# Performance work log

Measured on AMD Instinct MI355X. Metric: run time of the kernel, lower is better.

## Reference

```python
import jax, jax.numpy as jnp
import numpy as np

T, H, E, K, I = 2048, 2048, 64, 8, 768
CAP = 512


def setup_inputs() -> dict:
    key = jax.random.key(0)
    ks = jax.random.split(key, 5)
    s = 0.02
    return {
        "hidden_states": jax.random.normal(ks[0], (T, H), jnp.float32),
        "w_router": jax.random.normal(ks[1], (E, H), jnp.float32) * s,
        "w_gate": jax.random.normal(ks[2], (E, H, I), jnp.float32) * s,
        "w_up": jax.random.normal(ks[3], (E, H, I), jnp.float32) * s,
        "w_down": jax.random.normal(ks[4], (E, I, H), jnp.float32) * s,
    }


def _moe(x, w_router, w_gate, w_up, w_down):
    Tn = x.shape[0]
    # --- router: softmax -> top-k -> renormalize (norm_topk_prob=True) ---
    logits = x @ w_router.T                                   # [T, E]
    probs = jax.nn.softmax(logits.astype(jnp.float32), axis=-1)
    topk_w, topk_idx = jax.lax.top_k(probs, K)                # [T, K]
    topk_w = topk_w / jnp.sum(topk_w, axis=-1, keepdims=True)
    # --- dispatch: sort (token, expert) pairs by expert, scatter into capacity buffers ---
    e = topk_idx.reshape(-1)                                  # [T*K] expert id per pair
    t = jnp.repeat(jnp.arange(Tn), K)                         # [T*K] token id per pair
    w = topk_w.reshape(-1)                                    # [T*K] combine weight per pair
    order = jnp.argsort(e, stable=True)
    e_s, t_s, w_s = e[order], t[order], w[order]
    counts = jax.ops.segment_sum(jnp.ones_like(e_s), e_s, num_segments=E)  # [E]
    starts = jnp.cumsum(counts) - counts                      # start offset of each expert group
    pos = jnp.arange(Tn * K) - starts[e_s]                    # slot within expert
    valid = pos < CAP
    posc = jnp.where(valid, pos, 0)
    vm = valid.astype(x.dtype)[:, None]
    buf = jnp.zeros((E, CAP, H), x.dtype).at[e_s, posc].add(x[t_s] * vm)   # [E, C, H]
    # --- grouped expert SwiGLU FFN: down(silu(gate(x)) * up(x)) ---
    g = jnp.einsum('ech,ehi->eci', buf, w_gate)               # [E, C, I]
    u = jnp.einsum('ech,ehi->eci', buf, w_up)                 # [E, C, I]
    y = jnp.einsum('eci,eih->ech', jax.nn.silu(g) * u, w_down)  # [E, C, H]
    # --- combine: gather expert outputs back to tokens, weighted sum ---
    gw = (w_s.astype(x.dtype) * valid.astype(x.dtype))[:, None]
    out = jnp.zeros((Tn, H), x.dtype).at[t_s].add(gw * y[e_s, posc])
    return out


def reference(hidden_states, w_router, w_gate, w_up, w_down):
    return _moe(hidden_states, w_router, w_gate, w_up, w_down)
```

## Files before the change

kernel.cpp:

```cpp
#include <hip/hip_runtime.h>
#include <hip/hip_bf16.h>
#include <math.h>

#define T_TOK 2048
#define H_DIM 2048
#define NEXP  64
#define TOPK  8
#define I_DIM 768
#define CAPE  512
#define MTMAX 4
#define LDW   40

typedef short bf16x8 __attribute__((ext_vector_type(8)));
typedef float f32x4  __attribute__((ext_vector_type(4)));

__device__ __forceinline__ unsigned short f2bf(float f) {
  unsigned u = __float_as_uint(f);
  u += 0x7fffu + ((u >> 16) & 1u);
  return (unsigned short)(u >> 16);
}
__device__ __forceinline__ float bf2f(unsigned short b) {
  return __uint_as_float(((unsigned)b) << 16);
}
__device__ __forceinline__ unsigned pack2(float lo, float hi) {
  __hip_bfloat162 h = __float22bfloat162_rn(make_float2(lo, hi));
  unsigned r; __builtin_memcpy(&r, &h, 4); return r;
}

__global__ __launch_bounds__(256) void k_xcvt(const float* __restrict__ x,
                                              unsigned short* __restrict__ xb) {
  const size_t i = ((size_t)blockIdx.x * 256 + threadIdx.x) * 8;
  float4 p = *(const float4*)(x + i);
  float4 q = *(const float4*)(x + i + 4);
  union { unsigned u[4]; bf16x8 v; } r;
  r.u[0] = pack2(p.x, p.y); r.u[1] = pack2(p.z, p.w);
  r.u[2] = pack2(q.x, q.y); r.u[3] = pack2(q.z, q.w);
  *(bf16x8*)(xb + i) = r.v;
}

__global__ __launch_bounds__(256) void k_router(const float* __restrict__ x,
                                                const float* __restrict__ wr,
                                                int* __restrict__ topk_idx,
                                                float* __restrict__ topk_w) {
  const int lane = threadIdx.x & 63;
  const int t = blockIdx.x * 4 + (threadIdx.x >> 6);
  const float4* xr   = (const float4*)(x + (size_t)t * H_DIM);
  const float4* wrow = (const float4*)(wr + (size_t)lane * H_DIM);
  float acc = 0.f;
  for (int i = 0; i < H_DIM / 4; ++i) {
    float4 a = xr[i], b = wrow[i];
    acc = fmaf(a.x, b.x, acc); acc = fmaf(a.y, b.y, acc);
    acc = fmaf(a.z, b.z, acc); acc = fmaf(a.w, b.w, acc);
  }
  float cur = acc;
  float val[TOPK]; int idx[TOPK];
#pragma unroll
  for (int r = 0; r < TOPK; ++r) {
    float bv = cur; int bi = lane;
#pragma unroll
    for (int off = 32; off > 0; off >>= 1) {
      float ov = __shfl_xor(bv, off);
      int   oi = __shfl_xor(bi, off);
      if (ov > bv || (ov == bv && oi < bi)) { bv = ov; bi = oi; }
    }
    val[r] = bv; idx[r] = bi;
    if (lane == bi) cur = -INFINITY;
  }
  float m = val[0], s = 0.f, w[TOPK];
#pragma unroll
  for (int r = 0; r < TOPK; ++r) { w[r] = expf(val[r] - m); s += w[r]; }
  if (lane < TOPK) {
    topk_idx[t * TOPK + lane] = idx[lane];
    topk_w [t * TOPK + lane] = w[lane] / s;
  }
}

__global__ __launch_bounds__(1024) void k_rank(const int* __restrict__ topk_idx,
                                               int* __restrict__ pair_pos,
                                               int* __restrict__ slot_token,
                                               int* __restrict__ cnts) {
  __shared__ int s_run[64];
  __shared__ int s_whist[16][64];
  const int tid = threadIdx.x, lane = tid & 63, wv = tid >> 6;
  const int sub = wv >> 2;
  if (tid < 64) s_run[tid] = 0;
  for (int it = 0; it < 16; ++it) {
    const int p = (it * 4 + sub) * 256 + (tid & 255);
    const int e = topk_idx[p];
    __syncthreads();
    s_whist[wv][lane] = 0;
    __syncthreads();
    unsigned long long m = ~0ull;
#pragma unroll
    for (int b = 0; b < 6; ++b) {
      unsigned long long bb = __ballot((e >> b) & 1);
      m &= ((e >> b) & 1) ? bb : ~bb;
    }
    const int rw = __popcll(m & ((1ull << lane) - 1ull));
    if (rw == 0) s_whist[wv][e] = __popcll(m);
    __syncthreads();
    int off = rw;
    for (int w2 = 0; w2 < wv; ++w2) off += s_whist[w2][e];
    const int pos = s_run[e] + off;
    pair_pos[p] = pos;
    if (pos < CAPE) slot_token[e * CAPE + pos] = p >> 3;
    __syncthreads();
    if (tid < 64) {
      int tsum = 0;
#pragma unroll
      for (int w2 = 0; w2 < 16; ++w2) tsum += s_whist[w2][tid];
      s_run[tid] += tsum;
    }
  }
  __syncthreads();
  if (tid < 64) cnts[tid] = s_run[tid];
}

__global__ __launch_bounds__(512) void k_gateup(const unsigned short* __restrict__ xb,
                                                const float* __restrict__ wg,
                                                const float* __restrict__ wu,
                                                const int* __restrict__ slot_token,
                                                const int* __restrict__ cnts,
                                                unsigned short* __restrict__ act) {
  const int NB = NEXP * MTMAX * 6;
  const int v = (blockIdx.x & 7) * (NB / 8) + (blockIdx.x >> 3);
  const int e = v / (MTMAX * 6);
  const int rem = v % (MTMAX * 6);
  const int mt = rem / 6, nt = rem % 6;

  int cnt = cnts[e]; cnt = cnt < CAPE ? cnt : CAPE;
  if (cnt <= 0 || mt * 128 >= cnt) return;
  const int m0 = mt << 7;

  __shared__ __align__(16) short As[2][128 * LDW];
  __shared__ __align__(16) short Bg[2][128 * LDW];
  __shared__ __align__(16) short Bu[2][128 * LDW];

  const int tid = threadIdx.x;
  const int lane = tid & 63, wave = tid >> 6;
  const int wm = wave >> 2, wn = wave & 3;
  const int lr = lane & 15, lg = lane >> 4;

  const int a_row = tid >> 2, a_ko = (tid & 3) * 8;
  const int b_mat = tid >> 8;
  const int b_idx = tid & 255;
  const int b_kq = b_idx & 7, b_nq = b_idx >> 3;
  const size_t wbase = (size_t)e * H_DIM * I_DIM + (size_t)nt * 128;

  const int tok = (m0 + a_row < cnt) ? slot_token[e * CAPE + m0 + a_row] : 0;
  const unsigned short* xr = xb + (size_t)tok * H_DIM + a_ko;
  const float* bp  = (b_mat ? wu : wg) + wbase + (size_t)(4 * b_kq) * I_DIM + 4 * b_nq;
  short* Bdst0 = b_mat ? Bu[0] : Bg[0];
  short* Bdst1 = b_mat ? Bu[1] : Bg[1];

  f32x4 accg[4][2], accu[4][2];
#pragma unroll
  for (int mi = 0; mi < 4; ++mi)
#pragma unroll
    for (int ni = 0; ni < 2; ++ni) {
      accg[mi][ni] = (f32x4){0.f, 0.f, 0.f, 0.f};
      accu[mi][ni] = (f32x4){0.f, 0.f, 0.f, 0.f};
    }

  struct Tile { bf16x8 a; float4 b[4]; };

  auto LOAD = [&](Tile& Tl, int kt) {
    const int k0 = kt * 32;
    Tl.a = *(const bf16x8*)(xr + k0);
    const float* r0 = bp + (size_t)k0 * I_DIM;
#pragma unroll
    for (int j = 0; j < 4; ++j)
      Tl.b[j] = *(const float4*)(r0 + (size_t)j * I_DIM);
  };
  auto STORE = [&](const Tile& Tl, int b) {
    *(bf16x8*)(&As[b][a_row * LDW + a_ko]) = Tl.a;
    short* Bd = b ? Bdst1 : Bdst0;
    const float* q0 = (const float*)&Tl.b[0];
    const float* q1 = (const float*)&Tl.b[1];
    const float* q2 = (const float*)&Tl.b[2];
    const float* q3 = (const float*)&Tl.b[3];
#pragma unroll
    for (int i = 0; i < 4; ++i) {
      uint2 w = { pack2(q0[i], q1[i]), pack2(q2[i], q3[i]) };
      *(uint2*)(&Bd[(4 * b_nq + i) * LDW + 4 * b_kq]) = w;
    }
  };
  auto COMPUTE = [&](int b) {
    bf16x8 a[4], bg[2], bu[2];
#pragma unroll
    for (int mi = 0; mi < 4; ++mi)
      a[mi] = *(const bf16x8*)(&As[b][(wm * 64 + mi * 16 + lr) * LDW + lg * 8]);
#pragma unroll
    for (int ni = 0; ni < 2; ++ni) {
      bg[ni] = *(const bf16x8*)(&Bg[b][(wn * 32 + ni * 16 + lr) * LDW + lg * 8]);
      bu[ni] = *(const bf16x8*)(&Bu[b][(wn * 32 + ni * 16 + lr) * LDW + lg * 8]);
    }
#pragma unroll
    for (int mi = 0; mi < 4; ++mi)
#pragma unroll
      for (int ni = 0; ni < 2; ++ni) {
        accg[mi][ni] = __builtin_amdgcn_mfma_f32_16x16x32_bf16(a[mi], bg[ni], accg[mi][ni], 0, 0, 0);
        accu[mi][ni] = __builtin_amdgcn_mfma_f32_16x16x32_bf16(a[mi], bu[ni], accu[mi][ni], 0, 0, 0);
      }
  };

  const int NK = H_DIM / 32;
  Tile tA, tB;
  LOAD(tA, 0);
  STORE(tA, 0);
  LOAD(tB, 1);
  __syncthreads();

  int t = 0;
#pragma unroll 1
  for (; t + 2 < NK; t += 2) {
    LOAD(tA, t + 2);
    COMPUTE(0);
    STORE(tB, 1);
    __syncthreads();
    LOAD(tB, t + 3);
    COMPUTE(1);
    STORE(tA, 0);
    __syncthreads();
  }
  COMPUTE(0);
  STORE(tB, 1);
  __syncthreads();
  COMPUTE(1);

#pragma unroll
  for (int mi = 0; mi < 4; ++mi)
#pragma unroll
    for (int ni = 0; ni < 2; ++ni)
#pragma unroll
      for (int r = 0; r < 4; ++r) {
        const int row = m0 + wm * 64 + mi * 16 + lg * 4 + r;
        const int col = nt * 128 + wn * 32 + ni * 16 + lr;
        const float g = accg[mi][ni][r], u = accu[mi][ni][r];
        const float vv = (g / (1.f + __expf(-g))) * u;
        act[(size_t)(e * CAPE + row) * I_DIM + col] = f2bf(vv);
      }
}

__global__ __launch_bounds__(512) void k_down(const unsigned short* __restrict__ act,
                                              const float* __restrict__ wd,
                                              const int* __restrict__ cnts,
                                              unsigned short* __restrict__ y) {
  const int NB = NEXP * MTMAX * 16;
  const int v = (blockIdx.x & 7) * (NB / 8) + (blockIdx.x >> 3);
  const int e = v / (MTMAX * 16);
  const int rem = v % (MTMAX * 16);
  const int mt = rem / 16, nt = rem % 16;

  int cnt = cnts[e]; cnt = cnt < CAPE ? cnt : CAPE;
  if (cnt <= 0 || mt * 128 >= cnt) return;
  const int m0 = mt << 7;

  __shared__ __align__(16) short As[2][128 * LDW];
  __shared__ __align__(16) short Bt[2][128 * LDW];

  const int tid = threadIdx.x;
  const int lane = tid & 63, wave = tid >> 6;
  const int wm = wave >> 2, wn = wave & 3;
  const int lr = lane & 15, lg = lane >> 4;

  const int role = tid >> 8;
  const int ridx = tid & 255;
  const int b_kq = ridx & 7, b_nq = ridx >> 3;
  const int a_row = ridx >> 1, a_half = ridx & 1;
  const size_t wbase = (size_t)e * I_DIM * H_DIM + (size_t)nt * 128;

  const unsigned short* ap = act + (size_t)(e * CAPE + m0 + a_row) * I_DIM + a_half * 16;
  const float* bp = wd + wbase + (size_t)(4 * b_kq) * H_DIM + 4 * b_nq;

  f32x4 acc[4][2];
#pragma unroll
  for (int mi = 0; mi < 4; ++mi)
#pragma unroll
    for (int ni = 0; ni < 2; ++ni) acc[mi][ni] = (f32x4){0.f, 0.f, 0.f, 0.f};

  struct Tile { bf16x8 a0, a1; float4 b[4]; };

  auto LOAD = [&](Tile& Tl, int kt) {
    const int k0 = kt * 32;
    if (role) {
      Tl.a0 = *(const bf16x8*)(ap + k0);
      Tl.a1 = *(const bf16x8*)(ap + k0 + 8);
    } else {
      const float* r0 = bp + (size_t)k0 * H_DIM;
#pragma unroll
      for (int j = 0; j < 4; ++j)
        Tl.b[j] = *(const float4*)(r0 + (size_t)j * H_DIM);
    }
  };
  auto STORE = [&](const Tile& Tl, int b) {
    if (role) {
      *(bf16x8*)(&As[b][a_row * LDW + a_half * 16])     = Tl.a0;
      *(bf16x8*)(&As[b][a_row * LDW + a_half * 16 + 8]) = Tl.a1;
    } else {
      const float* q0 = (const float*)&Tl.b[0];
      const float* q1 = (const float*)&Tl.b[1];
      const float* q2 = (const float*)&Tl.b[2];
      const float* q3 = (const float*)&Tl.b[3];
#pragma unroll
      for (int i = 0; i < 4; ++i) {
        uint2 w = { pack2(q0[i], q1[i]), pack2(q2[i], q3[i]) };
        *(uint2*)(&Bt[b][(4 * b_nq + i) * LDW + 4 * b_kq]) = w;
      }
    }
  };
  auto COMPUTE = [&](int b) {
    bf16x8 a[4], bb[2];
#pragma unroll
    for (int mi = 0; mi < 4; ++mi)
      a[mi] = *(const bf16x8*)(&As[b][(wm * 64 + mi * 16 + lr) * LDW + lg * 8]);
#pragma unroll
    for (int ni = 0; ni < 2; ++ni)
      bb[ni] = *(const bf16x8*)(&Bt[b][(wn * 32 + ni * 16 + lr) * LDW + lg * 8]);
#pragma unroll
    for (int mi = 0; mi < 4; ++mi)
#pragma unroll
      for (int ni = 0; ni < 2; ++ni)
        acc[mi][ni] = __builtin_amdgcn_mfma_f32_16x16x32_bf16(a[mi], bb[ni], acc[mi][ni], 0, 0, 0);
  };

  const int NK = I_DIM / 32;
  Tile tA, tB;
  LOAD(tA, 0);
  STORE(tA, 0);
  LOAD(tB, 1);
  __syncthreads();

  int t = 0;
#pragma unroll 1
  for (; t + 2 < NK; t += 2) {
    LOAD(tA, t + 2);
    COMPUTE(0);
    STORE(tB, 1);
    __syncthreads();
    LOAD(tB, t + 3);
    COMPUTE(1);
    STORE(tA, 0);
    __syncthreads();
  }
  COMPUTE(0);
  STORE(tB, 1);
  __syncthreads();
  COMPUTE(1);

#pragma unroll
  for (int mi = 0; mi < 4; ++mi)
#pragma unroll
    for (int ni = 0; ni < 2; ++ni)
#pragma unroll
      for (int r = 0; r < 4; ++r) {
        const int row = m0 + wm * 64 + mi * 16 + lg * 4 + r;
        const int col = nt * 128 + wn * 32 + ni * 16 + lr;
        y[(size_t)(e * CAPE + row) * H_DIM + col] = f2bf(acc[mi][ni][r]);
      }
}

__global__ __launch_bounds__(256) void k_combine(const unsigned short* __restrict__ y,
                                                 const int* __restrict__ topk_idx,
                                                 const float* __restrict__ topk_w,
                                                 const int* __restrict__ pair_pos,
                                                 float* __restrict__ out) {
  const int t = blockIdx.x;
  __shared__ int s_e[TOPK]; __shared__ int s_p[TOPK]; __shared__ float s_w[TOPK];
  if (threadIdx.x < TOPK) {
    s_e[threadIdx.x] = topk_idx[t * TOPK + threadIdx.x];
    s_p[threadIdx.x] = pair_pos[t * TOPK + threadIdx.x];
    s_w[threadIdx.x] = topk_w [t * TOPK + threadIdx.x];
  }
  __syncthreads();
  const int h0 = threadIdx.x * 8;
  float acc[8] = {0.f, 0.f, 0.f, 0.f, 0.f, 0.f, 0.f, 0.f};
#pragma unroll
  for (int k = 0; k < TOPK; ++k) {
    const int pos = s_p[k];
    if (pos >= CAPE) continue;
    const float w = s_w[k];
    const bf16x8 vv = *(const bf16x8*)(&y[(size_t)(s_e[k] * CAPE + pos) * H_DIM + h0]);
#pragma unroll
    for (int j = 0; j < 8; ++j) acc[j] += w * bf2f((unsigned short)vv[j]);
  }
  float4 o0 = {acc[0], acc[1], acc[2], acc[3]};
  float4 o1 = {acc[4], acc[5], acc[6], acc[7]};
  *(float4*)(out + (size_t)t * H_DIM + h0)     = o0;
  *(float4*)(out + (size_t)t * H_DIM + h0 + 4) = o1;
}

extern "C" void kernel_launch(void* const* d_in, const int* in_sizes, int n_in,
                              void* d_out, int out_size, void* d_ws, size_t ws_size,
                              hipStream_t stream) {
  const float* x   = (const float*)d_in[0];
  const float* wr  = (const float*)d_in[1];
  const float* wgt = (const float*)d_in[2];
  const float* wup = (const float*)d_in[3];
  const float* wdn = (const float*)d_in[4];
  float* out = (float*)d_out;

  char* ws = (char*)d_ws;
  int*            topk_idx   = (int*)(ws);
  float*          topk_w     = (float*)(ws + 65536);
  int*            pair_pos   = (int*)(ws + 131072);
  int*            cnts       = (int*)(ws + 196608);
  int*            slot_token = (int*)(ws + 196864);
  unsigned short* xb         = (unsigned short*)(ws + 327936);
  unsigned short* act        = (unsigned short*)(ws + 327936 + 8388608);
  unsigned short* yb         = (unsigned short*)(ws + 327936 + 8388608 + 50331648);

  k_xcvt   <<<dim3(T_TOK * H_DIM / 2048), dim3(256), 0, stream>>>(x, xb);
  k_router <<<dim3(T_TOK / 4),        dim3(256), 0, stream>>>(x, wr, topk_idx, topk_w);
  k_rank   <<<dim3(1),                dim3(1024), 0, stream>>>(topk_idx, pair_pos, slot_token, cnts);
  k_gateup <<<dim3(NEXP * MTMAX * 6), dim3(512), 0, stream>>>(xb, wgt, wup, slot_token, cnts, act);
  k_down   <<<dim3(NEXP * MTMAX * 16),dim3(512), 0, stream>>>(act, wdn, cnts, yb);
  k_combine<<<dim3(T_TOK),            dim3(256), 0, stream>>>(yb, topk_idx, topk_w, pair_pos, out);
}
```

Before: 733.3 us.

## Load gate/up A operands directly into registers and batch router tokens per wave

The gate/up kernel no longer stages the gathered token rows through shared memory. Each lane now loads its MFMA A fragments straight from global memory, one step ahead of use, which removes the A-tile LDS writes and reads and halves part of the shared footprint. The cost is redundant global and L2 traffic, since the four column-waves fetch the same rows, plus more register pressure. Separately, the router gives each wave four tokens so every w_router load is reused four times, and the grid is cut to a quarter.

```diff
diff --git a/kernel.cpp b/kernel.cpp
--- a/kernel.cpp
+++ b/kernel.cpp
@@ -43,35 +43,44 @@
                                                 int* __restrict__ topk_idx,
                                                 float* __restrict__ topk_w) {
   const int lane = threadIdx.x & 63;
-  const int t = blockIdx.x * 4 + (threadIdx.x >> 6);
-  const float4* xr   = (const float4*)(x + (size_t)t * H_DIM);
+  const int t0 = blockIdx.x * 16 + (threadIdx.x >> 6) * 4;
   const float4* wrow = (const float4*)(wr + (size_t)lane * H_DIM);
-  float acc = 0.f;
+  const float4* xr0 = (const float4*)(x + (size_t)(t0 + 0) * H_DIM);
+  const float4* xr1 = (const float4*)(x + (size_t)(t0 + 1) * H_DIM);
+  const float4* xr2 = (const float4*)(x + (size_t)(t0 + 2) * H_DIM);
+  const float4* xr3 = (const float4*)(x + (size_t)(t0 + 3) * H_DIM);
+  float acc[4] = {0.f, 0.f, 0.f, 0.f};
   for (int i = 0; i < H_DIM / 4; ++i) {
-    float4 a = xr[i], b = wrow[i];
-    acc = fmaf(a.x, b.x, acc); acc = fmaf(a.y, b.y, acc);
-    acc = fmaf(a.z, b.z, acc); acc = fmaf(a.w, b.w, acc);
-  }
-  float cur = acc;
-  float val[TOPK]; int idx[TOPK];
-#pragma unroll
-  for (int r = 0; r < TOPK; ++r) {
-    float bv = cur; int bi = lane;
-#pragma unroll
-    for (int off = 32; off > 0; off >>= 1) {
-      float ov = __shfl_xor(bv, off);
-      int   oi = __shfl_xor(bi, off);
-      if (ov > bv || (ov == bv && oi < bi)) { bv = ov; bi = oi; }
-    }
-    val[r] = bv; idx[r] = bi;
-    if (lane == bi) cur = -INFINITY;
-  }
-  float m = val[0], s = 0.f, w[TOPK];
-#pragma unroll
-  for (int r = 0; r < TOPK; ++r) { w[r] = expf(val[r] - m); s += w[r]; }
-  if (lane < TOPK) {
-    topk_idx[t * TOPK + lane] = idx[lane];
-    topk_w [t * TOPK + lane] = w[lane] / s;
+    float4 b = wrow[i];
+    float4 a0 = xr0[i], a1 = xr1[i], a2 = xr2[i], a3 = xr3[i];
+    acc[0] = fmaf(a0.x,b.x,fmaf(a0.y,b.y,fmaf(a0.z,b.z,fmaf(a0.w,b.w,acc[0]))));
+    acc[1] = fmaf(a1.x,b.x,fmaf(a1.y,b.y,fmaf(a1.z,b.z,fmaf(a1.w,b.w,acc[1]))));
+    acc[2] = fmaf(a2.x,b.x,fmaf(a2.y,b.y,fmaf(a2.z,b.z,fmaf(a2.w,b.w,acc[2]))));
+    acc[3] = fmaf(a3.x,b.x,fmaf(a3.y,b.y,fmaf(a3.z,b.z,fmaf(a3.w,b.w,acc[3]))));
+  }
+#pragma unroll
+  for (int j = 0; j < 4; ++j) {
+    float cur = acc[j];
+    float val[TOPK]; int idx[TOPK];
+#pragma unroll
+    for (int r = 0; r < TOPK; ++r) {
+      float bv = cur; int bi = lane;
+#pragma unroll
+      for (int off = 32; off > 0; off >>= 1) {
+        float ov = __shfl_xor(bv, off);
+        int   oi = __shfl_xor(bi, off);
+        if (ov > bv || (ov == bv && oi < bi)) { bv = ov; bi = oi; }
+      }
+      val[r] = bv; idx[r] = bi;
+      if (lane == bi) cur = -INFINITY;
+    }
+    float m = val[0], s = 0.f, w[TOPK];
+#pragma unroll
+    for (int r = 0; r < TOPK; ++r) { w[r] = expf(val[r] - m); s += w[r]; }
+    if (lane < TOPK) {
+      topk_idx[(t0 + j) * TOPK + lane] = idx[lane];
+      topk_w [(t0 + j) * TOPK + lane] = w[lane] / s;
+    }
   }
 }
 
@@ -132,7 +141,6 @@
   if (cnt <= 0 || mt * 128 >= cnt) return;
   const int m0 = mt << 7;
 
-  __shared__ __align__(16) short As[2][128 * LDW];
   __shared__ __align__(16) short Bg[2][128 * LDW];
   __shared__ __align__(16) short Bu[2][128 * LDW];
 
@@ -141,14 +149,18 @@
   const int wm = wave >> 2, wn = wave & 3;
   const int lr = lane & 15, lg = lane >> 4;
 
-  const int a_row = tid >> 2, a_ko = (tid & 3) * 8;
+  const unsigned short* axp[4];
+#pragma unroll
+  for (int mi = 0; mi < 4; ++mi) {
+    const int row = m0 + wm * 64 + mi * 16 + lr;
+    const int tok = (row < cnt) ? slot_token[e * CAPE + row] : 0;
+    axp[mi] = xb + (size_t)tok * H_DIM + lg * 8;
+  }
+
   const int b_mat = tid >> 8;
   const int b_idx = tid & 255;
   const int b_kq = b_idx & 7, b_nq = b_idx >> 3;
   const size_t wbase = (size_t)e * H_DIM * I_DIM + (size_t)nt * 128;
-
-  const int tok = (m0 + a_row < cnt) ? slot_token[e * CAPE + m0 + a_row] : 0;
-  const unsigned short* xr = xb + (size_t)tok * H_DIM + a_ko;
   const float* bp  = (b_mat ? wu : wg) + wbase + (size_t)(4 * b_kq) * I_DIM + 4 * b_nq;
   short* Bdst0 = b_mat ? Bu[0] : Bg[0];
   short* Bdst1 = b_mat ? Bu[1] : Bg[1];
@@ -162,18 +174,23 @@
       accu[mi][ni] = (f32x4){0.f, 0.f, 0.f, 0.f};
     }
 
-  struct Tile { bf16x8 a; float4 b[4]; };
-
+  struct Tile { float4 b[4]; };
+  Tile tA, tB;
+  bf16x8 aC[4], aN[4];
+
+  auto ALOADR = [&](bf16x8* dst, int kt) {
+    const int k0 = kt * 32;
+#pragma unroll
+    for (int mi = 0; mi < 4; ++mi)
+      dst[mi] = *(const bf16x8*)(axp[mi] + k0);
+  };
   auto LOAD = [&](Tile& Tl, int kt) {
-    const int k0 = kt * 32;
-    Tl.a = *(const bf16x8*)(xr + k0);
-    const float* r0 = bp + (size_t)k0 * I_DIM;
+    const float* r0 = bp + (size_t)(kt * 32) * I_DIM;
 #pragma unroll
     for (int j = 0; j < 4; ++j)
       Tl.b[j] = *(const float4*)(r0 + (size_t)j * I_DIM);
   };
   auto STORE = [&](const Tile& Tl, int b) {
-    *(bf16x8*)(&As[b][a_row * LDW + a_ko]) = Tl.a;
     short* Bd = b ? Bdst1 : Bdst0;
     const float* q0 = (const float*)&Tl.b[0];
     const float* q1 = (const float*)&Tl.b[1];
@@ -185,11 +202,8 @@
       *(uint2*)(&Bd[(4 * b_nq + i) * LDW + 4 * b_kq]) = w;
     }
   };
-  auto COMPUTE = [&](int b) {
-    bf16x8 a[4], bg[2], bu[2];
-#pragma unroll
-    for (int mi = 0; mi < 4; ++mi)
-      a[mi] = *(const bf16x8*)(&As[b][(wm * 64 + mi * 16 + lr) * LDW + lg * 8]);
+  auto COMPUTE = [&](int b, const bf16x8* a) {
+    bf16x8 bg[2], bu[2];
 #pragma unroll
     for (int ni = 0; ni < 2; ++ni) {
       bg[ni] = *(const bf16x8*)(&Bg[b][(wn * 32 + ni * 16 + lr) * LDW + lg * 8]);
@@ -205,28 +219,31 @@
   };
 
   const int NK = H_DIM / 32;
-  Tile tA, tB;
   LOAD(tA, 0);
   STORE(tA, 0);
   LOAD(tB, 1);
+  ALOADR(aC, 0);
   __syncthreads();
 
   int t = 0;
 #pragma unroll 1
   for (; t + 2 < NK; t += 2) {
     LOAD(tA, t + 2);
-    COMPUTE(0);
+    ALOADR(aN, t + 1);
+    COMPUTE(0, aC);
     STORE(tB, 1);
     __syncthreads();
     LOAD(tB, t + 3);
-    COMPUTE(1);
+    ALOADR(aC, t + 2);
+    COMPUTE(1, aN);
     STORE(tA, 0);
     __syncthreads();
   }
-  COMPUTE(0);
+  ALOADR(aN, NK - 1);
+  COMPUTE(0, aC);
   STORE(tB, 1);
   __syncthreads();
-  COMPUTE(1);
+  COMPUTE(1, aN);
 
 #pragma unroll
   for (int mi = 0; mi < 4; ++mi)
@@ -411,7 +428,7 @@
   unsigned short* yb         = (unsigned short*)(ws + 327936 + 8388608 + 50331648);
 
   k_xcvt   <<<dim3(T_TOK * H_DIM / 2048), dim3(256), 0, stream>>>(x, xb);
-  k_router <<<dim3(T_TOK / 4),        dim3(256), 0, stream>>>(x, wr, topk_idx, topk_w);
+  k_router <<<dim3(T_TOK / 16),       dim3(256), 0, stream>>>(x, wr, topk_idx, topk_w);
   k_rank   <<<dim3(1),                dim3(1024), 0, stream>>>(topk_idx, pair_pos, slot_token, cnts);
   k_gateup <<<dim3(NEXP * MTMAX * 6), dim3(512), 0, stream>>>(xb, wgt, wup, slot_token, cnts, act);
   k_down   <<<dim3(NEXP * MTMAX * 16),dim3(512), 0, stream>>>(act, wdn, cnts, yb);
```

After: 877.3 us. 19.6% more time.
